# Optimization experiments

Measured on AMD Instinct MI355X. Metric: run time of the kernel, lower is better.

The kernel has to match this reference:

```python
import jax, jax.numpy as jnp
import numpy as np

N_NODES = 100000
N_EDGES = 1600000


def _spmm(row, col, val, x, n):
    # out[i] = sum_{e: row[e]==i} val[e] * x[col[e]]  (sparse adj @ dense x)
    return jax.ops.segment_sum(val[:, None] * x[col], row, num_segments=n)


def setup_inputs() -> dict:
    key = jax.random.key(0)
    ks = jax.random.split(key, 6)
    x = jax.random.normal(ks[0], (N_NODES, 128), dtype=jnp.float32)
    edge_row = jnp.sort(jax.random.randint(ks[1], (N_EDGES,), 0, N_NODES, dtype=jnp.int64))
    edge_col = jax.random.randint(ks[2], (N_EDGES,), 0, N_NODES, dtype=jnp.int64)
    # glorot-initialized linear layers (pyg Linear with weight_initializer='glorot')
    W0 = jax.random.normal(ks[3], (128, 128), dtype=jnp.float32) * np.sqrt(2.0 / (128 + 128))
    b0 = jnp.zeros((128,), dtype=jnp.float32)
    W1 = jax.random.normal(ks[4], (128, 64), dtype=jnp.float32) * np.sqrt(2.0 / (128 + 64))
    b1 = jnp.zeros((64,), dtype=jnp.float32)
    return {"x": x, "edge_row": edge_row, "edge_col": edge_col,
            "W0": W0, "b0": b0, "W1": W1, "b1": b1}


def reference(x, edge_row, edge_col, W0, b0, W1, b1):
    n = x.shape[0]
    # adj_norm: symmetric GCN normalization D^{-1/2} A D^{-1/2}
    ones = jnp.ones(edge_row.shape[0], dtype=x.dtype)
    deg = jax.ops.segment_sum(ones, edge_row, num_segments=n)
    dinv = jnp.where(deg > 0, jax.lax.rsqrt(jnp.maximum(deg, 1.0)), 0.0).astype(x.dtype)
    val = dinv[edge_row] * dinv[edge_col]
    # layer 0: linear -> SpMM -> relu (dropout is a no-op in inference/eval)
    h = x @ W0 + b0
    h = _spmm(edge_row, edge_col, val, h, n)
    h = jax.nn.relu(h)
    # layer 1: linear -> SpMM
    h = h @ W1 + b1
    h = _spmm(edge_row, edge_col, val, h, n)
    return jax.nn.log_softmax(h, axis=-1)
```

## Files before the change

kernel.cpp:

```cpp
#include <hip/hip_runtime.h>
#include <hip/hip_bf16.h>

#define NN 100000
#define NE 1600000

typedef __bf16 bf16x8 __attribute__((ext_vector_type(8)));
typedef float  f32x4  __attribute__((ext_vector_type(4)));

__global__ __launch_bounds__(256) void prep_kernel(const int* __restrict__ row,
                                                   int* __restrict__ row_ptr,
                                                   const float* __restrict__ W0,
                                                   const float* __restrict__ W1,
                                                   __hip_bfloat16* __restrict__ Wt0,
                                                   __hip_bfloat16* __restrict__ Wt1) {
    int b = blockIdx.x;
    if (b < NE / 256) {
        int e = b * 256 + threadIdx.x;
        int r  = row[e];
        int rp = (e == 0) ? -1 : row[e - 1];
        for (int i = rp + 1; i <= r; ++i) row_ptr[i] = e;
        if (e == NE - 1) {
            for (int i = r + 1; i <= NN; ++i) row_ptr[i] = NE;
        }
    } else {
        int idx = (b - NE / 256) * 256 + threadIdx.x;
        if (idx < 128 * 128) {
            int n = idx >> 7, k = idx & 127;
            Wt0[idx] = __float2bfloat16(W0[(size_t)k * 128 + n]);
        } else {
            int r2 = idx - 128 * 128;
            int n = r2 >> 7, k = r2 & 127;
            Wt1[r2] = __float2bfloat16(W1[(size_t)k * 64 + n]);
        }
    }
}

__device__ inline float deg_scale(const int* __restrict__ row_ptr, int i) {
    int dg = row_ptr[i + 1] - row_ptr[i];
    return (dg > 0) ? rsqrtf((float)dg) : 0.0f;
}

template <int NO, typename InT>
__global__ __launch_bounds__(512) void gemm_mfma(const InT* __restrict__ X,
                                                 const __hip_bfloat16* __restrict__ Wt,
                                                 const float* __restrict__ bias,
                                                 const int* __restrict__ row_ptr,
                                                 __hip_bfloat16* __restrict__ out, int M) {
    constexpr int NT = NO / 16;
    __shared__ unsigned short Ws[NO * 128];
    __shared__ unsigned short Cs[128 * 128];

    const int t = threadIdx.x;
    const int w = t >> 6, lane = t & 63;
    const int l15 = lane & 15, quad = lane >> 4;
    const int rbase = blockIdx.x * 128;

    for (int i = t; i < NO * 16; i += 512) {
        int n = i >> 4, g = i & 15;
        *(uint4*)&Ws[n * 128 + ((g ^ (n & 7)) << 3)] = ((const uint4*)Wt)[i];
    }
    __syncthreads();

    const int arow_g = rbase + w * 16 + l15;
    const int arow   = (arow_g < M) ? arow_g : (M - 1);

    bf16x8 af[4];
    if constexpr (sizeof(InT) == 4) {
        float4 lo[4], hi[4];
#pragma unroll
        for (int kc = 0; kc < 4; ++kc) {
            const float4* src = (const float4*)&X[(size_t)arow * 128 + kc * 32 + quad * 8];
            lo[kc] = src[0];
            hi[kc] = src[1];
        }
#pragma unroll
        for (int kc = 0; kc < 4; ++kc) {
            union { bf16x8 v; __hip_bfloat162 h[4]; } u;
            u.h[0] = __float22bfloat162_rn(make_float2(lo[kc].x, lo[kc].y));
            u.h[1] = __float22bfloat162_rn(make_float2(lo[kc].z, lo[kc].w));
            u.h[2] = __float22bfloat162_rn(make_float2(hi[kc].x, hi[kc].y));
            u.h[3] = __float22bfloat162_rn(make_float2(hi[kc].z, hi[kc].w));
            af[kc] = u.v;
        }
    } else {
        union { bf16x8 v; uint4 q; } u[4];
#pragma unroll
        for (int kc = 0; kc < 4; ++kc)
            u[kc].q = *(const uint4*)&X[(size_t)arow * 128 + kc * 32 + quad * 8];
#pragma unroll
        for (int kc = 0; kc < 4; ++kc) af[kc] = u[kc].v;
    }

    f32x4 acc[NT];
#pragma unroll
    for (int nt = 0; nt < NT; ++nt) {
        float bv = bias[nt * 16 + l15];
        acc[nt][0] = bv; acc[nt][1] = bv; acc[nt][2] = bv; acc[nt][3] = bv;
    }

#pragma unroll
    for (int kc = 0; kc < 4; ++kc) {
#pragma unroll
        for (int nt = 0; nt < NT; ++nt) {
            int brow = nt * 16 + l15;
            bf16x8 bfr = *(const bf16x8*)&Ws[brow * 128 + (((kc * 4 + quad) ^ (brow & 7)) << 3)];
            acc[nt] = __builtin_amdgcn_mfma_f32_16x16x32_bf16(af[kc], bfr, acc[nt], 0, 0, 0);
        }
    }

    __hip_bfloat16* Cp = (__hip_bfloat16*)Cs;
#pragma unroll
    for (int r4 = 0; r4 < 4; ++r4) {
        int lrow = w * 16 + quad * 4 + r4;
        int grow = rbase + lrow;
        float sc = (grow < M) ? deg_scale(row_ptr, grow) : 0.f;
#pragma unroll
        for (int nt = 0; nt < NT; ++nt) {
            int ct = nt * 16 + l15;
            Cp[lrow * 128 + ((((ct >> 3) ^ (lrow & 7)) << 3)) + (ct & 7)] =
                __float2bfloat16(acc[nt][r4] * sc);
        }
    }
    constexpr int RJ  = NO / 8;
    constexpr int CNT = (16 * RJ) / 64;
#pragma unroll
    for (int k = 0; k < CNT; ++k) {
        int idx = k * 64 + lane;
        int lr16 = idx / RJ, j = idx % RJ;
        int lrow = w * 16 + lr16;
        int grow = rbase + lrow;
        if (grow < M) {
            uint4 v = *(const uint4*)&Cp[lrow * 128 + ((j ^ (lrow & 7)) << 3)];
            *(uint4*)&out[(size_t)grow * NO + (j << 3)] = v;
        }
    }
}

__global__ __launch_bounds__(256) void spmm_relu_128(const int* __restrict__ row_ptr,
                                                     const int* __restrict__ col,
                                                     const unsigned int* __restrict__ H,
                                                     __hip_bfloat16* __restrict__ out, int N) {
    const int lane = threadIdx.x & 63;
    int i = __builtin_amdgcn_readfirstlane(blockIdx.x * 4 + (threadIdx.x >> 6));
    if (i >= N) return;
    const int e0 = __builtin_amdgcn_readfirstlane(row_ptr[i]);
    const int e1 = __builtin_amdgcn_readfirstlane(row_ptr[i + 1]);
    const int dg = e1 - e0;
    const float di = (dg > 0) ? rsqrtf((float)dg) : 0.0f;
    float accx = 0.f, accy = 0.f;
    int e = e0;
    for (; e + 16 <= e1; e += 16) {
        unsigned int u[16];
#pragma unroll
        for (int j = 0; j < 16; ++j) {
            int c = __builtin_amdgcn_readfirstlane(col[e + j]);
            u[j] = H[(size_t)c * 64 + lane];
        }
#pragma unroll
        for (int j = 0; j < 16; ++j) {
            accx += __uint_as_float(u[j] << 16);
            accy += __uint_as_float(u[j] & 0xffff0000u);
        }
    }
    for (; e + 8 <= e1; e += 8) {
        unsigned int u[8];
#pragma unroll
        for (int j = 0; j < 8; ++j) {
            int c = __builtin_amdgcn_readfirstlane(col[e + j]);
            u[j] = H[(size_t)c * 64 + lane];
        }
#pragma unroll
        for (int j = 0; j < 8; ++j) {
            accx += __uint_as_float(u[j] << 16);
            accy += __uint_as_float(u[j] & 0xffff0000u);
        }
    }
    for (; e < e1; ++e) {
        int c = __builtin_amdgcn_readfirstlane(col[e]);
        unsigned int u = H[(size_t)c * 64 + lane];
        accx += __uint_as_float(u << 16);
        accy += __uint_as_float(u & 0xffff0000u);
    }
    accx = fmaxf(accx * di, 0.f);
    accy = fmaxf(accy * di, 0.f);
    *(__hip_bfloat162*)&out[(size_t)i * 128 + 2 * lane] =
        __float22bfloat162_rn(make_float2(accx, accy));
}

__global__ __launch_bounds__(256) void spmm_logsoftmax_64(const int* __restrict__ row_ptr,
                                                          const int* __restrict__ col,
                                                          const unsigned short* __restrict__ H,
                                                          float* __restrict__ out, int N) {
    const int lane = threadIdx.x & 63;
    int i = __builtin_amdgcn_readfirstlane(blockIdx.x * 4 + (threadIdx.x >> 6));
    if (i >= N) return;
    const int e0 = __builtin_amdgcn_readfirstlane(row_ptr[i]);
    const int e1 = __builtin_amdgcn_readfirstlane(row_ptr[i + 1]);
    const int dg = e1 - e0;
    const float di = (dg > 0) ? rsqrtf((float)dg) : 0.0f;
    float acc = 0.f;
    int e = e0;
    for (; e + 16 <= e1; e += 16) {
        unsigned short u[16];
#pragma unroll
        for (int j = 0; j < 16; ++j) {
            int c = __builtin_amdgcn_readfirstlane(col[e + j]);
            u[j] = H[(size_t)c * 64 + lane];
        }
#pragma unroll
        for (int j = 0; j < 16; ++j)
            acc += __uint_as_float((unsigned int)u[j] << 16);
    }
    for (; e + 8 <= e1; e += 8) {
        unsigned short u[8];
#pragma unroll
        for (int j = 0; j < 8; ++j) {
            int c = __builtin_amdgcn_readfirstlane(col[e + j]);
            u[j] = H[(size_t)c * 64 + lane];
        }
#pragma unroll
        for (int j = 0; j < 8; ++j)
            acc += __uint_as_float((unsigned int)u[j] << 16);
    }
    for (; e < e1; ++e) {
        int c = __builtin_amdgcn_readfirstlane(col[e]);
        acc += __uint_as_float((unsigned int)H[(size_t)c * 64 + lane] << 16);
    }
    acc *= di;
    float m = acc;
#pragma unroll
    for (int off = 32; off > 0; off >>= 1)
        m = fmaxf(m, __shfl_xor(m, off, 64));
    float ex = __expf(acc - m);
    float s = ex;
#pragma unroll
    for (int off = 32; off > 0; off >>= 1)
        s += __shfl_xor(s, off, 64);
    out[(size_t)i * 64 + lane] = acc - m - __logf(s);
}

extern "C" void kernel_launch(void* const* d_in, const int* in_sizes, int n_in,
                              void* d_out, int out_size, void* d_ws, size_t ws_size,
                              hipStream_t stream) {
    const float* x    = (const float*)d_in[0];
    const int*   erow = (const int*)d_in[1];
    const int*   ecol = (const int*)d_in[2];
    const float* W0   = (const float*)d_in[3];
    const float* b0   = (const float*)d_in[4];
    const float* W1   = (const float*)d_in[5];
    const float* b1   = (const float*)d_in[6];
    float* out = (float*)d_out;

    char* ws = (char*)d_ws;
    int*             row_ptr = (int*)ws;
    __hip_bfloat16*  h0b     = (__hip_bfloat16*)(ws + (1u << 20));
    __hip_bfloat16*  h1b     = (__hip_bfloat16*)(ws + 27000000u);
    __hip_bfloat16*  h2b     = (__hip_bfloat16*)(ws + 53000000u);
    __hip_bfloat16*  Wt0     = (__hip_bfloat16*)(ws + 66000000u);
    __hip_bfloat16*  Wt1     = (__hip_bfloat16*)(ws + 66100000u);

    prep_kernel<<<NE / 256 + 96, 256, 0, stream>>>(erow, row_ptr, W0, W1, Wt0, Wt1);
    gemm_mfma<128, float><<<(NN + 127) / 128, 512, 0, stream>>>(x, Wt0, b0, row_ptr, h0b, NN);
    spmm_relu_128<<<(NN + 3) / 4, 256, 0, stream>>>(row_ptr, ecol,
                                                    (const unsigned int*)h0b, h1b, NN);
    gemm_mfma<64, __hip_bfloat16><<<(NN + 127) / 128, 512, 0, stream>>>(h1b, Wt1, b1, row_ptr, h2b, NN);
    spmm_logsoftmax_64<<<(NN + 3) / 4, 256, 0, stream>>>(row_ptr, ecol,
                                                         (const unsigned short*)h2b, out, NN);
}
```

Before: 239.2 us.

## Fuse layer-0 SpMM+ReLU with layer-1 GEMM via shared-memory tile

Combines the first sparse aggregation (with ReLU) and the following 128x64 linear layer into one kernel. Each 512-thread block aggregates 32 rows into a swizzled LDS tile, then runs bf16 MFMA against the LDS-staged W1 and writes the degree-scaled result directly. This drops one kernel launch and the write and re-read of the 128-wide intermediate activation. In exchange, each block reloads W1 into LDS, the block size and LDS use change occupancy, and the grid assumes NN is divisible by 32.

```diff
diff --git a/kernel.cpp b/kernel.cpp
--- a/kernel.cpp
+++ b/kernel.cpp
@@ -136,55 +136,100 @@
     }
 }
 
-__global__ __launch_bounds__(256) void spmm_relu_128(const int* __restrict__ row_ptr,
-                                                     const int* __restrict__ col,
-                                                     const unsigned int* __restrict__ H,
-                                                     __hip_bfloat16* __restrict__ out, int N) {
-    const int lane = threadIdx.x & 63;
-    int i = __builtin_amdgcn_readfirstlane(blockIdx.x * 4 + (threadIdx.x >> 6));
-    if (i >= N) return;
-    const int e0 = __builtin_amdgcn_readfirstlane(row_ptr[i]);
-    const int e1 = __builtin_amdgcn_readfirstlane(row_ptr[i + 1]);
-    const int dg = e1 - e0;
-    const float di = (dg > 0) ? rsqrtf((float)dg) : 0.0f;
-    float accx = 0.f, accy = 0.f;
-    int e = e0;
-    for (; e + 16 <= e1; e += 16) {
-        unsigned int u[16];
-#pragma unroll
-        for (int j = 0; j < 16; ++j) {
-            int c = __builtin_amdgcn_readfirstlane(col[e + j]);
-            u[j] = H[(size_t)c * 64 + lane];
-        }
-#pragma unroll
-        for (int j = 0; j < 16; ++j) {
-            accx += __uint_as_float(u[j] << 16);
-            accy += __uint_as_float(u[j] & 0xffff0000u);
-        }
-    }
-    for (; e + 8 <= e1; e += 8) {
-        unsigned int u[8];
-#pragma unroll
-        for (int j = 0; j < 8; ++j) {
-            int c = __builtin_amdgcn_readfirstlane(col[e + j]);
-            u[j] = H[(size_t)c * 64 + lane];
-        }
-#pragma unroll
-        for (int j = 0; j < 8; ++j) {
-            accx += __uint_as_float(u[j] << 16);
-            accy += __uint_as_float(u[j] & 0xffff0000u);
-        }
-    }
-    for (; e < e1; ++e) {
-        int c = __builtin_amdgcn_readfirstlane(col[e]);
-        unsigned int u = H[(size_t)c * 64 + lane];
-        accx += __uint_as_float(u << 16);
-        accy += __uint_as_float(u & 0xffff0000u);
-    }
-    accx = fmaxf(accx * di, 0.f);
-    accy = fmaxf(accy * di, 0.f);
-    *(__hip_bfloat162*)&out[(size_t)i * 128 + 2 * lane] =
-        __float22bfloat162_rn(make_float2(accx, accy));
+__global__ __launch_bounds__(512) void spmm_relu_gemm1(const int* __restrict__ row_ptr,
+                                                       const int* __restrict__ col,
+                                                       const unsigned int* __restrict__ H,
+                                                       const __hip_bfloat16* __restrict__ Wt1,
+                                                       const float* __restrict__ b1,
+                                                       __hip_bfloat16* __restrict__ out) {
+    __shared__ unsigned short As[32 * 128];
+    __shared__ unsigned short Ws[64 * 128];
+
+    const int t = threadIdx.x;
+    const int w = t >> 6, lane = t & 63;
+    const int l15 = lane & 15, quad = lane >> 4;
+    const int rbase = blockIdx.x * 32;
+
+    for (int i = t; i < 64 * 16; i += 512) {
+        int n = i >> 4, g = i & 15;
+        *(uint4*)&Ws[n * 128 + ((g ^ (n & 7)) << 3)] = ((const uint4*)Wt1)[i];
+    }
+
+    const int gsw = ((lane >> 2) << 3) + ((lane & 3) << 1);
+#pragma unroll 1
+    for (int rr = 0; rr < 4; ++rr) {
+        const int il = w * 4 + rr;
+        const int i  = rbase + il;
+        const int e0 = __builtin_amdgcn_readfirstlane(row_ptr[i]);
+        const int e1 = __builtin_amdgcn_readfirstlane(row_ptr[i + 1]);
+        const int dg = e1 - e0;
+        const float di = (dg > 0) ? rsqrtf((float)dg) : 0.0f;
+        float accx = 0.f, accy = 0.f;
+        int e = e0;
+        for (; e + 16 <= e1; e += 16) {
+            unsigned int u[16];
+#pragma unroll
+            for (int j = 0; j < 16; ++j) {
+                int c = __builtin_amdgcn_readfirstlane(col[e + j]);
+                u[j] = H[(size_t)c * 64 + lane];
+            }
+#pragma unroll
+            for (int j = 0; j < 16; ++j) {
+                accx += __uint_as_float(u[j] << 16);
+                accy += __uint_as_float(u[j] & 0xffff0000u);
+            }
+        }
+        for (; e + 8 <= e1; e += 8) {
+            unsigned int u[8];
+#pragma unroll
+            for (int j = 0; j < 8; ++j) {
+                int c = __builtin_amdgcn_readfirstlane(col[e + j]);
+                u[j] = H[(size_t)c * 64 + lane];
+            }
+#pragma unroll
+            for (int j = 0; j < 8; ++j) {
+                accx += __uint_as_float(u[j] << 16);
+                accy += __uint_as_float(u[j] & 0xffff0000u);
+            }
+        }
+        for (; e < e1; ++e) {
+            int c = __builtin_amdgcn_readfirstlane(col[e]);
+            unsigned int u = H[(size_t)c * 64 + lane];
+            accx += __uint_as_float(u << 16);
+            accy += __uint_as_float(u & 0xffff0000u);
+        }
+        accx = fmaxf(accx * di, 0.f);
+        accy = fmaxf(accy * di, 0.f);
+        union { __hip_bfloat162 h; unsigned int uu; } p;
+        p.h = __float22bfloat162_rn(make_float2(accx, accy));
+        *(unsigned int*)&As[il * 128 + ((((lane >> 2) ^ (il & 7)) << 3) + ((lane & 3) << 1))] = p.uu;
+    }
+    __syncthreads();
+
+    const int rb = (w & 1) * 16;
+    const int cb = (w >> 1) * 16;
+    const int arow_l = rb + l15;
+    const int asw = arow_l & 7;
+
+    f32x4 acc;
+    {
+        float bv = b1[cb + l15];
+        acc[0] = bv; acc[1] = bv; acc[2] = bv; acc[3] = bv;
+    }
+#pragma unroll
+    for (int kc = 0; kc < 4; ++kc) {
+        bf16x8 af = *(const bf16x8*)&As[arow_l * 128 + (((kc * 4 + quad) ^ asw) << 3)];
+        int brow = cb + l15;
+        bf16x8 bfr = *(const bf16x8*)&Ws[brow * 128 + (((kc * 4 + quad) ^ (brow & 7)) << 3)];
+        acc = __builtin_amdgcn_mfma_f32_16x16x32_bf16(af, bfr, acc, 0, 0, 0);
+    }
+
+#pragma unroll
+    for (int r4 = 0; r4 < 4; ++r4) {
+        int grow = rbase + rb + quad * 4 + r4;
+        float sc = deg_scale(row_ptr, grow);
+        out[(size_t)grow * 64 + cb + l15] = __float2bfloat16(acc[r4] * sc);
+    }
 }
 
 __global__ __launch_bounds__(256) void spmm_logsoftmax_64(const int* __restrict__ row_ptr,
@@ -254,16 +299,14 @@
     char* ws = (char*)d_ws;
     int*             row_ptr = (int*)ws;
     __hip_bfloat16*  h0b     = (__hip_bfloat16*)(ws + (1u << 20));
-    __hip_bfloat16*  h1b     = (__hip_bfloat16*)(ws + 27000000u);
-    __hip_bfloat16*  h2b     = (__hip_bfloat16*)(ws + 53000000u);
-    __hip_bfloat16*  Wt0     = (__hip_bfloat16*)(ws + 66000000u);
-    __hip_bfloat16*  Wt1     = (__hip_bfloat16*)(ws + 66100000u);
+    __hip_bfloat16*  h2b     = (__hip_bfloat16*)(ws + 27000000u);
+    __hip_bfloat16*  Wt0     = (__hip_bfloat16*)(ws + 41000000u);
+    __hip_bfloat16*  Wt1     = (__hip_bfloat16*)(ws + 41100000u);
 
     prep_kernel<<<NE / 256 + 96, 256, 0, stream>>>(erow, row_ptr, W0, W1, Wt0, Wt1);
     gemm_mfma<128, float><<<(NN + 127) / 128, 512, 0, stream>>>(x, Wt0, b0, row_ptr, h0b, NN);
-    spmm_relu_128<<<(NN + 3) / 4, 256, 0, stream>>>(row_ptr, ecol,
-                                                    (const unsigned int*)h0b, h1b, NN);
-    gemm_mfma<64, __hip_bfloat16><<<(NN + 127) / 128, 512, 0, stream>>>(h1b, Wt1, b1, row_ptr, h2b, NN);
+    spmm_relu_gemm1<<<NN / 32, 512, 0, stream>>>(row_ptr, ecol,
+                                                 (const unsigned int*)h0b, Wt1, b1, h2b);
     spmm_logsoftmax_64<<<(NN + 3) / 4, 256, 0, stream>>>(row_ptr, ecol,
                                                          (const unsigned short*)h2b, out, NN);
 }
```

Measured after the change: 237.7 us. About the same (-0.6%).
